# Kernel optimization log

Measured on AMD Instinct MI355X. Metric: run time of the kernel, lower is better.

Reference implementation:

```python
import jax, jax.numpy as jnp
import numpy as np

B, C_IN, C_OUT, H, W = 8, 32, 32, 256, 256
M1H, M2H = 32, 32  # modes1//2, modes2//2 (dilate=1)
WSCALE = 0.02      # ~xavier-ish scale for weights


def setup_inputs() -> dict:
    key = jax.random.key(0)
    ks = jax.random.split(key, 6)
    wshape = (C_IN, C_OUT, M1H, M2H)
    return {
        "x": jax.random.normal(ks[0], (B, C_IN, H, W), jnp.float32),
        "w1r": jax.random.normal(ks[1], wshape, jnp.float32) * WSCALE,
        "w1i": jax.random.normal(ks[2], wshape, jnp.float32) * WSCALE,
        "w2r": jax.random.normal(ks[3], wshape, jnp.float32) * WSCALE,
        "w2i": jax.random.normal(ks[4], wshape, jnp.float32) * WSCALE,
        "bias": jax.random.normal(ks[5], (1, C_OUT, 1, 1), jnp.float32),
    }


def reference(x, w1r, w1i, w2r, w2i, bias):
    # complex spectral weights (torch.view_as_complex equivalent)
    w1 = w1r + 1j * w1i  # [I, O, m1h, m2h]
    w2 = w2r + 1j * w2i
    b, c, h, w = x.shape
    x_ft = jnp.fft.rfft2(x)  # [B, I, H, W//2+1] complex64
    # mode-truncated complex channel mixing on low-frequency corners
    out_lo = jnp.einsum('bixy,ioxy->boxy', x_ft[:, :, :M1H, :M2H], w1)
    out_hi = jnp.einsum('bixy,ioxy->boxy', x_ft[:, :, -M1H:, :M2H], w2)
    out_ft = jnp.zeros((b, w1.shape[1], h, w // 2 + 1), jnp.complex64)
    out_ft = out_ft.at[:, :, :M1H, :M2H].set(out_lo)
    out_ft = out_ft.at[:, :, -M1H:, :M2H].set(out_hi)
    out = jnp.fft.irfft2(out_ft, s=(h, w))  # [B, O, H, W] float32
    return out + bias
```

## Files before the change

### kernel.cpp

```cpp
#include <hip/hip_runtime.h>
#include <hip/hip_bf16.h>


#define BD 256

typedef __attribute__((ext_vector_type(8))) short bf16x8;
typedef __attribute__((ext_vector_type(4))) float f32x4;

__device__ inline unsigned short f2bf(float f) {
    union { float f; unsigned u; } v; v.f = f;
    unsigned r = v.u + 0x7FFF + ((v.u >> 16) & 1);
    return (unsigned short)(r >> 16);
}

__global__ void k_setup(float2* __restrict__ tw,
                        unsigned short* __restrict__ BmA, unsigned short* __restrict__ BmC,
                        const float* __restrict__ w1r, const float* __restrict__ w1i,
                        const float* __restrict__ w2r, const float* __restrict__ w2i,
                        float2* __restrict__ wpack) {
    __shared__ float Tr[64][65];
    __shared__ float Ti[64][65];
    int b = blockIdx.x, t = threadIdx.x;
    if (b == 0) {
        double th = 6.283185307179586476925286766559 * (double)t / 256.0;
        tw[t] = make_float2((float)cos(th), (float)sin(th));
    } else if (b <= 128) {
        int idx = (b - 1) * BD + t;
        if (idx < 16384) {
            int w = idx & 255, n = idx >> 8;
            int ky = n >> 1, c = n & 1;
            double th = 6.283185307179586476925286766559 * (double)((ky * w) & 255) / 256.0;
            BmA[idx] = f2bf(c ? (float)(-sin(th)) : (float)cos(th));
        } else {
            int j = idx - 16384;
            int k = j & 63, w = j >> 6;
            int ky = k >> 1, c = k & 1;
            double th = 6.283185307179586476925286766559 * (double)((ky * w) & 255) / 256.0;
            BmC[j] = f2bf(c ? (float)(-sin(th)) : (float)cos(th));
        }
    } else {
        int blk = b - 129;
        int half = blk >> 8;
        int tile = blk & 255;
        int tr = tile >> 4, tc = tile & 15;
        int io0 = tr * 64, cm0 = tc * 64;
        const float* wr = half ? w2r : w1r;
        const float* wi = half ? w2i : w1i;
        int rr = t >> 2, c0 = (t & 3) * 16;
        {
            const float4* srcr = (const float4*)(wr + (long)(io0 + rr) * 1024 + cm0 + c0);
            const float4* srci = (const float4*)(wi + (long)(io0 + rr) * 1024 + cm0 + c0);
#pragma unroll
            for (int p = 0; p < 4; ++p) {
                float4 vr = srcr[p], vi = srci[p];
                int cc = c0 + p * 4;
                Tr[rr][cc + 0] = vr.x; Tr[rr][cc + 1] = vr.y; Tr[rr][cc + 2] = vr.z; Tr[rr][cc + 3] = vr.w;
                Ti[rr][cc + 0] = vi.x; Ti[rr][cc + 1] = vi.y; Ti[rr][cc + 2] = vi.z; Ti[rr][cc + 3] = vi.w;
            }
        }
        __syncthreads();
        {
            int cm = cm0 + rr;
            int ky = cm & 31;
            float s = (ky == 0 ? 1.0f : 2.0f) * (1.0f / 65536.0f);
            float2* dst = wpack + ((long)(half * 1024 + cm)) * 1024 + io0 + c0;
#pragma unroll
            for (int k = 0; k < 16; ++k)
                dst[k] = make_float2(Tr[c0 + k][rr] * s, Ti[c0 + k][rr] * s);
        }
    }
}

__global__ __launch_bounds__(512) void k_fftA(const float* __restrict__ x,
                                              const unsigned short* __restrict__ BmA,
                                              const float2* __restrict__ tw,
                                              float2* __restrict__ Z) {
    __shared__ __align__(16) unsigned short Bs[64 * 264];
    __shared__ __align__(16) unsigned short As[32 * 264];
    __shared__ __align__(16) float Ys[32 * 64];
    int t = threadIdx.x, bi = blockIdx.x >> 1, hh2 = blockIdx.x & 1;
    {
        int n = t >> 3, c0 = (t & 7) * 32;
        const uint4* src = (const uint4*)(BmA + n * 256 + c0);
        unsigned short* dst = &Bs[n * 264 + c0];
#pragma unroll
        for (int j = 0; j < 4; ++j) *(uint4*)(dst + j * 8) = src[j];
    }
    int sr = t >> 4, sc = (t & 15) * 16;
    const float* xrow = x + ((long)bi * 256 + hh2 * 128 + sr) * 256 + sc;
    float4 xb[4];
#pragma unroll
    for (int j = 0; j < 4; ++j) xb[j] = *(const float4*)(xrow + j * 4);
    {
        unsigned short* dst = &As[sr * 264 + sc];
#pragma unroll
        for (int j = 0; j < 4; ++j) {
            float4 v = xb[j]; ushort4 bq;
            bq.x = f2bf(v.x); bq.y = f2bf(v.y); bq.z = f2bf(v.z); bq.w = f2bf(v.w);
            *(ushort4*)(dst + j * 4) = bq;
        }
    }
    __syncthreads();
    int wv = t >> 6, lane = t & 63, lm = lane & 15, quad = lane >> 4;
    int mh = wv & 1, nq = wv >> 1;
    int kxi = t & 63, g = wv;
    int kxv = (kxi < 32) ? kxi : kxi + 192;
    float2 st = tw[kxv];
    float C = st.x, S = st.y;
    float zr[4] = {0.f, 0.f, 0.f, 0.f}, zi[4] = {0.f, 0.f, 0.f, 0.f};
    for (int c2 = 0; c2 < 4; ++c2) {
        f32x4 acc = {};
#pragma unroll
        for (int kk = 0; kk < 8; ++kk) {
            bf16x8 af = *(const bf16x8*)&As[(mh * 16 + lm) * 264 + kk * 32 + quad * 8];
            bf16x8 bf = *(const bf16x8*)&Bs[(nq * 16 + lm) * 264 + kk * 32 + quad * 8];
            acc = __builtin_amdgcn_mfma_f32_16x16x32_bf16(af, bf, acc, 0, 0, 0);
        }
        if (c2 < 3) {
            const float* xr = xrow + (c2 + 1) * 32 * 256;
#pragma unroll
            for (int j = 0; j < 4; ++j) xb[j] = *(const float4*)(xr + j * 4);
        }
#pragma unroll
        for (int r = 0; r < 4; ++r)
            Ys[(mh * 16 + quad * 4 + r) * 64 + nq * 16 + lm] = acc[r];
        __syncthreads();
        int gc = hh2 * 4 + c2;
        float2 cw = tw[(kxv * (gc * 32)) & 255];
        float cr = cw.x, ci = cw.y;
        for (int hh = 0; hh < 32; ++hh) {
            float4 y0 = *(const float4*)&Ys[hh * 64 + g * 8];
            float4 y1 = *(const float4*)&Ys[hh * 64 + g * 8 + 4];
            zr[0] = fmaf(y0.x, cr, fmaf(y0.y,  ci, zr[0]));
            zi[0] = fmaf(y0.y, cr, fmaf(-y0.x, ci, zi[0]));
            zr[1] = fmaf(y0.z, cr, fmaf(y0.w,  ci, zr[1]));
            zi[1] = fmaf(y0.w, cr, fmaf(-y0.z, ci, zi[1]));
            zr[2] = fmaf(y1.x, cr, fmaf(y1.y,  ci, zr[2]));
            zi[2] = fmaf(y1.y, cr, fmaf(-y1.x, ci, zi[2]));
            zr[3] = fmaf(y1.z, cr, fmaf(y1.w,  ci, zr[3]));
            zi[3] = fmaf(y1.w, cr, fmaf(-y1.z, ci, zi[3]));
            float nc = fmaf(cr, C, -ci * S);
            ci = fmaf(ci, C, cr * S);
            cr = nc;
        }
        if (c2 < 3) {
            unsigned short* dst = &As[sr * 264 + sc];
#pragma unroll
            for (int j = 0; j < 4; ++j) {
                float4 v = xb[j]; ushort4 bq;
                bq.x = f2bf(v.x); bq.y = f2bf(v.y); bq.z = f2bf(v.z); bq.w = f2bf(v.w);
                *(ushort4*)(dst + j * 4) = bq;
            }
        }
        __syncthreads();
    }
    float2* Zo = (float2*)As;
    {
#pragma unroll
        for (int j = 0; j < 4; ++j)
            Zo[kxi * 32 + g * 4 + j] = make_float2(zr[j], zi[j]);
    }
    __syncthreads();
    {
        float4* dst = (float4*)(Z + (long)(hh2 * 256 + bi) * 2048);
        const float4* src = (const float4*)Zo;
        dst[t] = src[t];
        dst[t + 512] = src[t + 512];
    }
}

__global__ void k_mix(const float2* __restrict__ Z, const float2* __restrict__ wpack,
                      float2* __restrict__ Zmix) {
    __shared__ float2 Ws[4][1024];
    __shared__ float2 Zs[256][4];
    __shared__ float2 Os[256][4];
    int t = threadIdx.x;
    int mk0 = blockIdx.x * 4;
    {
        const float4* src = (const float4*)(wpack + (long)mk0 * 1024);
        float4* dst = (float4*)&Ws[0][0];
        for (int j = t; j < 2048; j += BD) dst[j] = src[j];
    }
    for (int j = t; j < 512; j += BD) {
        int bi = j >> 1, p = j & 1;
        float4 a = *(const float4*)&Z[(long)bi * 2048 + mk0 + p * 2];
        float4 b = *(const float4*)&Z[(long)(256 + bi) * 2048 + mk0 + p * 2];
        float4 s;
        s.x = a.x + b.x; s.y = a.y + b.y; s.z = a.z + b.z; s.w = a.w + b.w;
        *(float4*)&Zs[bi][p * 2] = s;
    }
    __syncthreads();
    int o = t & 31, kk = (t >> 5) & 3, bh = t >> 7;
    float ar[4], ai[4];
#pragma unroll
    for (int j = 0; j < 4; ++j) { ar[j] = 0.f; ai[j] = 0.f; }
    for (int i = 0; i < 32; ++i) {
        float2 w = Ws[kk][i * 32 + o];
#pragma unroll
        for (int j = 0; j < 4; ++j) {
            float2 z = Zs[(bh * 4 + j) * 32 + i][kk];
            ar[j] = fmaf(z.x, w.x, fmaf(-z.y, w.y, ar[j]));
            ai[j] = fmaf(z.x, w.y, fmaf( z.y, w.x, ai[j]));
        }
    }
#pragma unroll
    for (int j = 0; j < 4; ++j)
        Os[(bh * 4 + j) * 32 + o][kk] = make_float2(ar[j], ai[j]);
    __syncthreads();
    for (int j = t; j < 512; j += BD) {
        int row = j >> 1, p = j & 1;
        *(float4*)&Zmix[(long)row * 2048 + mk0 + p * 2] = *(float4*)&Os[row][p * 2];
    }
}

__global__ __launch_bounds__(512) void k_fftC(const float2* __restrict__ Zmix,
                                              const float2* __restrict__ tw,
                                              const unsigned short* __restrict__ BmC,
                                              const float* __restrict__ bias,
                                              float* __restrict__ out) {
    __shared__ __align__(16) unsigned short Gs[128 * 72];
    __shared__ __align__(16) char buf[128 * 72 * 2];
    int t = threadIdx.x;
    int bo = blockIdx.x >> 1, hb = blockIdx.x & 1;
    float2* Zs = (float2*)buf;
    unsigned short* Bsh = (unsigned short*)buf;
    {
        const float4* src = (const float4*)(Zmix + (long)bo * 2048);
        float4* dst = (float4*)Zs;
        dst[t] = src[t];
        dst[t + 512] = src[t + 512];
    }
    __syncthreads();
    int h1 = t & 127, yh = t >> 7;
    int h = hb * 128 + h1;
    float2 st = tw[h];
    float C = st.x, S = st.y;
    float gr[8], gi[8];
#pragma unroll
    for (int k = 0; k < 8; ++k) { gr[k] = 0.f; gi[k] = 0.f; }
    float cr = 1.f, ci = 0.f;
    for (int hf = 0; hf < 2; ++hf) {
        if (hf) { float2 s2 = tw[(224 * h) & 255]; cr = s2.x; ci = s2.y; }
        for (int mm = 0; mm < 32; ++mm) {
            int m = hf * 32 + mm;
#pragma unroll
            for (int kk = 0; kk < 4; ++kk) {
                float4 z = *(const float4*)&Zs[m * 32 + yh * 8 + kk * 2];
                gr[kk*2]   = fmaf(z.x, cr, fmaf(-z.y, ci, gr[kk*2]));
                gi[kk*2]   = fmaf(z.y, cr, fmaf( z.x, ci, gi[kk*2]));
                gr[kk*2+1] = fmaf(z.z, cr, fmaf(-z.w, ci, gr[kk*2+1]));
                gi[kk*2+1] = fmaf(z.w, cr, fmaf( z.z, ci, gi[kk*2+1]));
            }
            float nc = fmaf(cr, C, -ci * S);
            ci = fmaf(ci, C, cr * S);
            cr = nc;
        }
    }
    {
        unsigned* Gp = (unsigned*)&Gs[h1 * 72 + yh * 16];
#pragma unroll
        for (int k = 0; k < 8; ++k)
            Gp[k] = (unsigned)f2bf(gr[k]) | ((unsigned)f2bf(gi[k]) << 16);
    }
    __syncthreads();
    int wv = t >> 6, lane = t & 63, m = lane & 15, quad = lane >> 4;
    bf16x8 a0 = *(const bf16x8*)&Gs[(wv * 16 + m) * 72 + quad * 8];
    bf16x8 a1 = *(const bf16x8*)&Gs[(wv * 16 + m) * 72 + 32 + quad * 8];
    float bv = bias[bo & 31];
    long rowbase = (long)bo * 256 + hb * 128 + wv * 16;
    for (int p = 0; p < 2; ++p) {
        if (p) __syncthreads();
        {
            int w = t >> 2, k0 = (t & 3) * 16;
            const uint4* src = (const uint4*)(BmC + (p * 128 + w) * 64 + k0);
            *(uint4*)&Bsh[w * 72 + k0]     = src[0];
            *(uint4*)&Bsh[w * 72 + k0 + 8] = src[1];
        }
        __syncthreads();
        f32x4 acc[8] = {};
#pragma unroll
        for (int nt = 0; nt < 8; ++nt) {
            bf16x8 b0 = *(const bf16x8*)&Bsh[(nt * 16 + m) * 72 + quad * 8];
            bf16x8 b1 = *(const bf16x8*)&Bsh[(nt * 16 + m) * 72 + 32 + quad * 8];
            acc[nt] = __builtin_amdgcn_mfma_f32_16x16x32_bf16(a0, b0, acc[nt], 0, 0, 0);
            acc[nt] = __builtin_amdgcn_mfma_f32_16x16x32_bf16(a1, b1, acc[nt], 0, 0, 0);
        }
#pragma unroll
        for (int nt = 0; nt < 8; ++nt)
#pragma unroll
            for (int r = 0; r < 4; ++r)
                out[(rowbase + quad * 4 + r) * 256 + p * 128 + nt * 16 + m] = acc[nt][r] + bv;
    }
}

extern "C" void kernel_launch(void* const* d_in, const int* in_sizes, int n_in,
                              void* d_out, int out_size, void* d_ws, size_t ws_size,
                              hipStream_t stream) {
    const float* x    = (const float*)d_in[0];
    const float* w1r  = (const float*)d_in[1];
    const float* w1i  = (const float*)d_in[2];
    const float* w2r  = (const float*)d_in[3];
    const float* w2i  = (const float*)d_in[4];
    const float* bias = (const float*)d_in[5];

    char* ws = (char*)d_ws;
    float2* tw             = (float2*)(ws);
    float2* wpack          = (float2*)(ws + 4096);
    unsigned short* BmA    = (unsigned short*)(ws + 4096 + (16l << 20));
    unsigned short* BmC    = BmA + 64 * 256;
    float2* Z              = (float2*)(ws + 4096 + (16l << 20) + 65536);
    float2* Zmix           = (float2*)((char*)Z + (8l << 20));
    float* out             = (float*)d_out;

    k_setup <<<1 + 128 + 512, BD, 0, stream>>>(tw, BmA, BmC, w1r, w1i, w2r, w2i, wpack);
    k_fftA  <<<512, 512, 0, stream>>>(x, BmA, tw, Z);
    k_mix   <<<512, BD, 0, stream>>>(Z, wpack, Zmix);
    k_fftC  <<<512, 512, 0, stream>>>(Zmix, tw, BmC, bias, out);
}
```

Baseline: 194.3 us.

## Replace scalar twiddle-recurrence H-axis DFTs with bf16 MFMA matmuls

The column (H-axis) DFT stages in both the forward and inverse kernels, which used scalar FMA loops with complex twiddle recurrences, are replaced by bf16 MFMA matrix multiplies against precomputed DFT matrices (Tm, Th) built in the setup kernel. The forward kernel now processes a whole 256-row image per block, so the split-half partial sums and their addition in the mix kernel go away and the Z buffer is halved. The intent is to move the remaining ALU-bound DFT work onto the matrix cores. In exchange, the intermediates are rounded to bf16, which lowers accuracy, and the forward kernel launches half as many blocks.

```diff
diff --git a/kernel.cpp b/kernel.cpp
--- a/kernel.cpp
+++ b/kernel.cpp
@@ -15,6 +15,7 @@
 
 __global__ void k_setup(float2* __restrict__ tw,
                         unsigned short* __restrict__ BmA, unsigned short* __restrict__ BmC,
+                        unsigned short* __restrict__ Tm, unsigned short* __restrict__ Th,
                         const float* __restrict__ w1r, const float* __restrict__ w1i,
                         const float* __restrict__ w2r, const float* __restrict__ w2i,
                         float2* __restrict__ wpack) {
@@ -38,8 +39,22 @@
             double th = 6.283185307179586476925286766559 * (double)((ky * w) & 255) / 256.0;
             BmC[j] = f2bf(c ? (float)(-sin(th)) : (float)cos(th));
         }
+    } else if (b <= 256) {
+        int idx = (b - 129) * BD + t;
+        int h = idx & 255, n2 = idx >> 8;
+        int j = n2 >> 1, c = n2 & 1;
+        int kx = (j < 32) ? j : j + 192;
+        double th = 6.283185307179586476925286766559 * (double)((kx * h) & 255) / 256.0;
+        Tm[idx] = f2bf(c ? (float)(-sin(th)) : (float)cos(th));
+    } else if (b <= 384) {
+        int idx = (b - 257) * BD + t;
+        int k2 = idx & 127, h = idx >> 7;
+        int m = k2 >> 1, c = k2 & 1;
+        int kx = (m < 32) ? m : m + 192;
+        double th = 6.283185307179586476925286766559 * (double)((kx * h) & 255) / 256.0;
+        Th[idx] = f2bf(c ? (float)(-sin(th)) : (float)cos(th));
     } else {
-        int blk = b - 129;
+        int blk = b - 385;
         int half = blk >> 8;
         int tile = blk & 255;
         int tr = tile >> 4, tc = tile & 15;
@@ -73,99 +88,76 @@
 
 __global__ __launch_bounds__(512) void k_fftA(const float* __restrict__ x,
                                               const unsigned short* __restrict__ BmA,
-                                              const float2* __restrict__ tw,
+                                              const unsigned short* __restrict__ Tm,
                                               float2* __restrict__ Z) {
-    __shared__ __align__(16) unsigned short Bs[64 * 264];
-    __shared__ __align__(16) unsigned short As[32 * 264];
-    __shared__ __align__(16) float Ys[32 * 64];
-    int t = threadIdx.x, bi = blockIdx.x >> 1, hh2 = blockIdx.x & 1;
-    {
-        int n = t >> 3, c0 = (t & 7) * 32;
-        const uint4* src = (const uint4*)(BmA + n * 256 + c0);
-        unsigned short* dst = &Bs[n * 264 + c0];
-#pragma unroll
-        for (int j = 0; j < 4; ++j) *(uint4*)(dst + j * 8) = src[j];
-    }
-    int sr = t >> 4, sc = (t & 15) * 16;
-    const float* xrow = x + ((long)bi * 256 + hh2 * 128 + sr) * 256 + sc;
-    float4 xb[4];
-#pragma unroll
-    for (int j = 0; j < 4; ++j) xb[j] = *(const float4*)(xrow + j * 4);
-    {
-        unsigned short* dst = &As[sr * 264 + sc];
-#pragma unroll
-        for (int j = 0; j < 4; ++j) {
-            float4 v = xb[j]; ushort4 bq;
-            bq.x = f2bf(v.x); bq.y = f2bf(v.y); bq.z = f2bf(v.z); bq.w = f2bf(v.w);
-            *(ushort4*)(dst + j * 4) = bq;
-        }
-    }
-    __syncthreads();
+    __shared__ __align__(16) unsigned short Ybt[64 * 264];
+    __shared__ __align__(16) char buf[64 * 264 * 2];
+    unsigned short* As = (unsigned short*)buf;
+    float* ZZs = (float*)buf;
+    int t = threadIdx.x, bi = blockIdx.x;
     int wv = t >> 6, lane = t & 63, lm = lane & 15, quad = lane >> 4;
-    int mh = wv & 1, nq = wv >> 1;
-    int kxi = t & 63, g = wv;
-    int kxv = (kxi < 32) ? kxi : kxi + 192;
-    float2 st = tw[kxv];
-    float C = st.x, S = st.y;
-    float zr[4] = {0.f, 0.f, 0.f, 0.f}, zi[4] = {0.f, 0.f, 0.f, 0.f};
-    for (int c2 = 0; c2 < 4; ++c2) {
-        f32x4 acc = {};
-#pragma unroll
-        for (int kk = 0; kk < 8; ++kk) {
-            bf16x8 af = *(const bf16x8*)&As[(mh * 16 + lm) * 264 + kk * 32 + quad * 8];
-            bf16x8 bf = *(const bf16x8*)&Bs[(nq * 16 + lm) * 264 + kk * 32 + quad * 8];
-            acc = __builtin_amdgcn_mfma_f32_16x16x32_bf16(af, bf, acc, 0, 0, 0);
-        }
-        if (c2 < 3) {
-            const float* xr = xrow + (c2 + 1) * 32 * 256;
-#pragma unroll
-            for (int j = 0; j < 4; ++j) xb[j] = *(const float4*)(xr + j * 4);
-        }
-#pragma unroll
-        for (int r = 0; r < 4; ++r)
-            Ys[(mh * 16 + quad * 4 + r) * 64 + nq * 16 + lm] = acc[r];
-        __syncthreads();
-        int gc = hh2 * 4 + c2;
-        float2 cw = tw[(kxv * (gc * 32)) & 255];
-        float cr = cw.x, ci = cw.y;
-        for (int hh = 0; hh < 32; ++hh) {
-            float4 y0 = *(const float4*)&Ys[hh * 64 + g * 8];
-            float4 y1 = *(const float4*)&Ys[hh * 64 + g * 8 + 4];
-            zr[0] = fmaf(y0.x, cr, fmaf(y0.y,  ci, zr[0]));
-            zi[0] = fmaf(y0.y, cr, fmaf(-y0.x, ci, zi[0]));
-            zr[1] = fmaf(y0.z, cr, fmaf(y0.w,  ci, zr[1]));
-            zi[1] = fmaf(y0.w, cr, fmaf(-y0.z, ci, zi[1]));
-            zr[2] = fmaf(y1.x, cr, fmaf(y1.y,  ci, zr[2]));
-            zi[2] = fmaf(y1.y, cr, fmaf(-y1.x, ci, zi[2]));
-            zr[3] = fmaf(y1.z, cr, fmaf(y1.w,  ci, zr[3]));
-            zi[3] = fmaf(y1.w, cr, fmaf(-y1.z, ci, zi[3]));
-            float nc = fmaf(cr, C, -ci * S);
-            ci = fmaf(ci, C, cr * S);
-            cr = nc;
-        }
-        if (c2 < 3) {
+    int nst = (wv >> 1) * 16, mh = wv & 1;
+    bf16x8 bfr[8];
+#pragma unroll
+    for (int kk = 0; kk < 8; ++kk)
+        bfr[kk] = *(const bf16x8*)&BmA[(nst + lm) * 256 + kk * 32 + quad * 8];
+    int sr = t >> 3, sc = (t & 7) * 32;
+    for (int c = 0; c < 4; ++c) {
+        {
+            const float* xp = x + ((long)bi * 256 + c * 64 + sr) * 256 + sc;
             unsigned short* dst = &As[sr * 264 + sc];
 #pragma unroll
-            for (int j = 0; j < 4; ++j) {
-                float4 v = xb[j]; ushort4 bq;
+            for (int j = 0; j < 8; ++j) {
+                float4 v = *(const float4*)(xp + j * 4);
+                ushort4 bq;
                 bq.x = f2bf(v.x); bq.y = f2bf(v.y); bq.z = f2bf(v.z); bq.w = f2bf(v.w);
                 *(ushort4*)(dst + j * 4) = bq;
             }
         }
         __syncthreads();
-    }
-    float2* Zo = (float2*)As;
-    {
-#pragma unroll
-        for (int j = 0; j < 4; ++j)
-            Zo[kxi * 32 + g * 4 + j] = make_float2(zr[j], zi[j]);
-    }
-    __syncthreads();
-    {
-        float4* dst = (float4*)(Z + (long)(hh2 * 256 + bi) * 2048);
-        const float4* src = (const float4*)Zo;
-        dst[t] = src[t];
-        dst[t + 512] = src[t + 512];
+        f32x4 acc0 = {}, acc1 = {};
+#pragma unroll
+        for (int kk = 0; kk < 8; ++kk) {
+            bf16x8 af0 = *(const bf16x8*)&As[(mh * 32 + lm) * 264 + kk * 32 + quad * 8];
+            bf16x8 af1 = *(const bf16x8*)&As[(mh * 32 + 16 + lm) * 264 + kk * 32 + quad * 8];
+            acc0 = __builtin_amdgcn_mfma_f32_16x16x32_bf16(af0, bfr[kk], acc0, 0, 0, 0);
+            acc1 = __builtin_amdgcn_mfma_f32_16x16x32_bf16(af1, bfr[kk], acc1, 0, 0, 0);
+        }
+        {
+            ushort4 w0, w1;
+            w0.x = f2bf(acc0[0]); w0.y = f2bf(acc0[1]); w0.z = f2bf(acc0[2]); w0.w = f2bf(acc0[3]);
+            w1.x = f2bf(acc1[0]); w1.y = f2bf(acc1[1]); w1.z = f2bf(acc1[2]); w1.w = f2bf(acc1[3]);
+            int base = (nst + lm) * 264 + c * 64 + mh * 32 + quad * 4;
+            *(ushort4*)&Ybt[base] = w0;
+            *(ushort4*)&Ybt[base + 16] = w1;
+        }
+        __syncthreads();
+    }
+    bf16x8 afr[8];
+#pragma unroll
+    for (int kk = 0; kk < 8; ++kk)
+        afr[kk] = *(const bf16x8*)&Tm[(wv * 16 + lm) * 256 + kk * 32 + quad * 8];
+    f32x4 az[4] = {};
+#pragma unroll
+    for (int kk = 0; kk < 8; ++kk)
+#pragma unroll
+        for (int nt = 0; nt < 4; ++nt) {
+            bf16x8 bf = *(const bf16x8*)&Ybt[(nt * 16 + lm) * 264 + kk * 32 + quad * 8];
+            az[nt] = __builtin_amdgcn_mfma_f32_16x16x32_bf16(afr[kk], bf, az[nt], 0, 0, 0);
+        }
+#pragma unroll
+    for (int nt = 0; nt < 4; ++nt)
+#pragma unroll
+        for (int r = 0; r < 4; ++r)
+            ZZs[(wv * 16 + quad * 4 + r) * 65 + nt * 16 + lm] = az[nt][r];
+    __syncthreads();
+#pragma unroll
+    for (int p = 0; p < 4; ++p) {
+        int cid = p * 512 + t;
+        int m = cid >> 5, ky = cid & 31;
+        float zr = ZZs[(2 * m) * 65 + 2 * ky]     - ZZs[(2 * m + 1) * 65 + 2 * ky + 1];
+        float zi = ZZs[(2 * m) * 65 + 2 * ky + 1] + ZZs[(2 * m + 1) * 65 + 2 * ky];
+        Z[(long)bi * 2048 + cid] = make_float2(zr, zi);
     }
 }
 
@@ -183,11 +175,7 @@
     }
     for (int j = t; j < 512; j += BD) {
         int bi = j >> 1, p = j & 1;
-        float4 a = *(const float4*)&Z[(long)bi * 2048 + mk0 + p * 2];
-        float4 b = *(const float4*)&Z[(long)(256 + bi) * 2048 + mk0 + p * 2];
-        float4 s;
-        s.x = a.x + b.x; s.y = a.y + b.y; s.z = a.z + b.z; s.w = a.w + b.w;
-        *(float4*)&Zs[bi][p * 2] = s;
+        *(float4*)&Zs[bi][p * 2] = *(const float4*)&Z[(long)bi * 2048 + mk0 + p * 2];
     }
     __syncthreads();
     int o = t & 31, kk = (t >> 5) & 3, bh = t >> 7;
@@ -214,58 +202,53 @@
 }
 
 __global__ __launch_bounds__(512) void k_fftC(const float2* __restrict__ Zmix,
-                                              const float2* __restrict__ tw,
+                                              const unsigned short* __restrict__ Th,
                                               const unsigned short* __restrict__ BmC,
                                               const float* __restrict__ bias,
                                               float* __restrict__ out) {
     __shared__ __align__(16) unsigned short Gs[128 * 72];
     __shared__ __align__(16) char buf[128 * 72 * 2];
+    unsigned short* Bz = (unsigned short*)buf;
+    unsigned short* Bsh = (unsigned short*)buf;
     int t = threadIdx.x;
     int bo = blockIdx.x >> 1, hb = blockIdx.x & 1;
-    float2* Zs = (float2*)buf;
-    unsigned short* Bsh = (unsigned short*)buf;
     {
-        const float4* src = (const float4*)(Zmix + (long)bo * 2048);
-        float4* dst = (float4*)Zs;
-        dst[t] = src[t];
-        dst[t + 512] = src[t + 512];
-    }
-    __syncthreads();
-    int h1 = t & 127, yh = t >> 7;
-    int h = hb * 128 + h1;
-    float2 st = tw[h];
-    float C = st.x, S = st.y;
-    float gr[8], gi[8];
-#pragma unroll
-    for (int k = 0; k < 8; ++k) { gr[k] = 0.f; gi[k] = 0.f; }
-    float cr = 1.f, ci = 0.f;
-    for (int hf = 0; hf < 2; ++hf) {
-        if (hf) { float2 s2 = tw[(224 * h) & 255]; cr = s2.x; ci = s2.y; }
-        for (int mm = 0; mm < 32; ++mm) {
-            int m = hf * 32 + mm;
-#pragma unroll
-            for (int kk = 0; kk < 4; ++kk) {
-                float4 z = *(const float4*)&Zs[m * 32 + yh * 8 + kk * 2];
-                gr[kk*2]   = fmaf(z.x, cr, fmaf(-z.y, ci, gr[kk*2]));
-                gi[kk*2]   = fmaf(z.y, cr, fmaf( z.x, ci, gi[kk*2]));
-                gr[kk*2+1] = fmaf(z.z, cr, fmaf(-z.w, ci, gr[kk*2+1]));
-                gi[kk*2+1] = fmaf(z.w, cr, fmaf( z.z, ci, gi[kk*2+1]));
+#pragma unroll
+        for (int p = 0; p < 4; ++p) {
+            int cid = p * 512 + t;
+            int m = cid >> 5, ky = cid & 31;
+            float2 z = Zmix[(long)bo * 2048 + cid];
+            unsigned short zr = f2bf(z.x), zi = f2bf(z.y), nzr = f2bf(-z.x);
+            Bz[(2 * ky) * 136 + 2 * m]         = zr;
+            Bz[(2 * ky) * 136 + 2 * m + 1]     = zi;
+            Bz[(2 * ky + 1) * 136 + 2 * m]     = zi;
+            Bz[(2 * ky + 1) * 136 + 2 * m + 1] = nzr;
+        }
+    }
+    __syncthreads();
+    int wv = t >> 6, lane = t & 63, lm = lane & 15, quad = lane >> 4;
+    {
+        bf16x8 afr[4];
+#pragma unroll
+        for (int kk = 0; kk < 4; ++kk)
+            afr[kk] = *(const bf16x8*)&Th[(hb * 128 + wv * 16 + lm) * 128 + kk * 32 + quad * 8];
+        f32x4 ag[4] = {};
+#pragma unroll
+        for (int kk = 0; kk < 4; ++kk)
+#pragma unroll
+            for (int nt = 0; nt < 4; ++nt) {
+                bf16x8 bf = *(const bf16x8*)&Bz[(nt * 16 + lm) * 136 + kk * 32 + quad * 8];
+                ag[nt] = __builtin_amdgcn_mfma_f32_16x16x32_bf16(afr[kk], bf, ag[nt], 0, 0, 0);
             }
-            float nc = fmaf(cr, C, -ci * S);
-            ci = fmaf(ci, C, cr * S);
-            cr = nc;
-        }
-    }
-    {
-        unsigned* Gp = (unsigned*)&Gs[h1 * 72 + yh * 16];
-#pragma unroll
-        for (int k = 0; k < 8; ++k)
-            Gp[k] = (unsigned)f2bf(gr[k]) | ((unsigned)f2bf(gi[k]) << 16);
-    }
-    __syncthreads();
-    int wv = t >> 6, lane = t & 63, m = lane & 15, quad = lane >> 4;
-    bf16x8 a0 = *(const bf16x8*)&Gs[(wv * 16 + m) * 72 + quad * 8];
-    bf16x8 a1 = *(const bf16x8*)&Gs[(wv * 16 + m) * 72 + 32 + quad * 8];
+#pragma unroll
+        for (int nt = 0; nt < 4; ++nt)
+#pragma unroll
+            for (int r = 0; r < 4; ++r)
+                Gs[(wv * 16 + quad * 4 + r) * 72 + nt * 16 + lm] = f2bf(ag[nt][r]);
+    }
+    __syncthreads();
+    bf16x8 a0 = *(const bf16x8*)&Gs[(wv * 16 + lm) * 72 + quad * 8];
+    bf16x8 a1 = *(const bf16x8*)&Gs[(wv * 16 + lm) * 72 + 32 + quad * 8];
     float bv = bias[bo & 31];
     long rowbase = (long)bo * 256 + hb * 128 + wv * 16;
     for (int p = 0; p < 2; ++p) {
@@ -280,8 +263,8 @@
         f32x4 acc[8] = {};
 #pragma unroll
         for (int nt = 0; nt < 8; ++nt) {
-            bf16x8 b0 = *(const bf16x8*)&Bsh[(nt * 16 + m) * 72 + quad * 8];
-            bf16x8 b1 = *(const bf16x8*)&Bsh[(nt * 16 + m) * 72 + 32 + quad * 8];
+            bf16x8 b0 = *(const bf16x8*)&Bsh[(nt * 16 + lm) * 72 + quad * 8];
+            bf16x8 b1 = *(const bf16x8*)&Bsh[(nt * 16 + lm) * 72 + 32 + quad * 8];
             acc[nt] = __builtin_amdgcn_mfma_f32_16x16x32_bf16(a0, b0, acc[nt], 0, 0, 0);
             acc[nt] = __builtin_amdgcn_mfma_f32_16x16x32_bf16(a1, b1, acc[nt], 0, 0, 0);
         }
@@ -289,7 +272,7 @@
         for (int nt = 0; nt < 8; ++nt)
 #pragma unroll
             for (int r = 0; r < 4; ++r)
-                out[(rowbase + quad * 4 + r) * 256 + p * 128 + nt * 16 + m] = acc[nt][r] + bv;
+                out[(rowbase + quad * 4 + r) * 256 + p * 128 + nt * 16 + lm] = acc[nt][r] + bv;
     }
 }
 
@@ -308,12 +291,14 @@
     float2* wpack          = (float2*)(ws + 4096);
     unsigned short* BmA    = (unsigned short*)(ws + 4096 + (16l << 20));
     unsigned short* BmC    = BmA + 64 * 256;
-    float2* Z              = (float2*)(ws + 4096 + (16l << 20) + 65536);
-    float2* Zmix           = (float2*)((char*)Z + (8l << 20));
+    unsigned short* Tm     = (unsigned short*)(ws + 4096 + (16l << 20) + 65536);
+    unsigned short* Th     = Tm + 128 * 256;
+    float2* Z              = (float2*)(ws + 4096 + (16l << 20) + 65536 + 131072);
+    float2* Zmix           = (float2*)((char*)Z + (4l << 20));
     float* out             = (float*)d_out;
 
-    k_setup <<<1 + 128 + 512, BD, 0, stream>>>(tw, BmA, BmC, w1r, w1i, w2r, w2i, wpack);
-    k_fftA  <<<512, 512, 0, stream>>>(x, BmA, tw, Z);
+    k_setup <<<897, BD, 0, stream>>>(tw, BmA, BmC, Tm, Th, w1r, w1i, w2r, w2i, wpack);
+    k_fftA  <<<256, 512, 0, stream>>>(x, BmA, Tm, Z);
     k_mix   <<<512, BD, 0, stream>>>(Z, wpack, Zmix);
-    k_fftC  <<<512, 512, 0, stream>>>(Zmix, tw, BmC, bias, out);
-}
+    k_fftC  <<<512, 512, 0, stream>>>(Zmix, Th, BmC, bias, out);
+}
```

After: 165.1 us. 1.18x faster.
